# Optimization experiments

Hardware: AMD Instinct MI355X
Metric: run time of the kernel (lower is better)

Reference implementation:

```python
import jax, jax.numpy as jnp
import numpy as np

N_USERS = 10000
N_ITEMS = 40000
HID = 64
NNZ = 2_000_000
B = 8192
N_TOT = N_USERS + N_ITEMS
HOP = 3


def setup_inputs() -> dict:
    key = jax.random.key(0)
    ks = jax.random.split(key, 13)
    emb = lambda k, n: jax.random.normal(k, (n, HID), dtype=jnp.float32) * (1.0 / np.sqrt(HID))
    # Dense social adjacency; scaled so repeated propagation stays numerically stable
    S = jax.random.uniform(ks[6], (N_USERS, N_USERS), dtype=jnp.float32) * (2.0 / N_USERS)
    return {
        "users": jax.random.randint(ks[0], (B,), 0, N_USERS),
        "pos": jax.random.randint(ks[1], (B,), 0, N_ITEMS),
        "neg": jax.random.randint(ks[2], (B,), 0, N_ITEMS),
        "user_embs": emb(ks[3], N_USERS),
        "item_embs": emb(ks[4], N_ITEMS),
        "user1_embs": emb(ks[5], N_USERS),
        "item1_embs": emb(ks[7], N_ITEMS),
        "user2_embs": emb(ks[8], N_USERS),
        "item2_embs": emb(ks[9], N_ITEMS),
        "S": S,
        "A_rows": jax.random.randint(ks[10], (NNZ,), 0, N_TOT, dtype=jnp.int32),
        "A_cols": jax.random.randint(ks[11], (NNZ,), 0, N_TOT, dtype=jnp.int32),
        "A_vals": jax.random.uniform(ks[12], (NNZ,), dtype=jnp.float32) * (1.0 / 40.0),
        "hop": HOP,
    }


def social_gcn(uemb, S, hop):
    # LightGCN-style propagation over dense social graph; mean over layers 0..hop
    h = uemb
    acc = uemb
    for _ in range(hop):
        h = S @ h                      # [n_users, hid] dense GEMM
        acc = acc + h
    return acc / (hop + 1)


def ui_gcn(uemb, iemb, rows, cols, vals, hop):
    # LightGCN over sparse bipartite user-item graph of size [N_TOT, N_TOT]
    ego = jnp.concatenate([uemb, iemb], axis=0)   # [N_TOT, hid]
    h = ego
    acc = ego
    for _ in range(hop):
        msgs = vals[:, None] * h[cols]            # gather + scale  [nnz, hid]
        h = jax.ops.segment_sum(msgs, rows, num_segments=N_TOT)
        acc = acc + h
    out = acc / (hop + 1)
    return out[:N_USERS], out[N_USERS:]


def reference(users, pos, neg, user_embs, item_embs, user1_embs, item1_embs,
              user2_embs, item2_embs, S, A_rows, A_cols, A_vals, hop):
    all_user_S = social_gcn(user_embs, S, hop)
    all_user_A, all_item = ui_gcn(user_embs, item_embs, A_rows, A_cols, A_vals, hop)
    all_user = 0.5 * all_user_S + 0.5 * all_user_A

    all_user_social = social_gcn(user1_embs, S, hop)
    all_item_social = item1_embs
    all_user_rating, all_item_rating = ui_gcn(user2_embs, item2_embs, A_rows, A_cols, A_vals, hop)

    return (all_user[users], all_item[pos], all_item[neg],
            all_user_S, all_user_A,
            all_user_social[users], all_item_social[pos], all_item_social[neg],
            all_user_rating[users], all_item_rating[pos], all_item_rating[neg])
```

## Files before the change

### kernel.cpp

```cpp
#include <hip/hip_runtime.h>

#define N_USERS 10000
#define N_ITEMS 40000
#define N_TOTAL 50000
#define HID     64
#define BATCH   8192
#define HOPS    3
#define KDIM    10000
#define KTILES  157
#define KPAD    (KTILES * 64)
#define MTILES  79
#define SPLITK  8
#define NSOC    (MTILES * SPLITK)

#define O0 0
#define O1 524288
#define O2 1048576
#define O3 1572864
#define O4 2212864
#define O5 2852864
#define O6 3377152
#define O7 3901440
#define O8 4425728
#define O9 4950016
#define O10 5474304

typedef __attribute__((ext_vector_type(8))) short short8;
typedef __attribute__((ext_vector_type(4))) float floatx4;

__device__ __forceinline__ unsigned short f32bf(float f) {
  union { float f; unsigned u; } v; v.f = f;
  unsigned r = v.u + 0x7fffu + ((v.u >> 16) & 1u);
  return (unsigned short)(r >> 16);
}

__device__ __forceinline__ short8 cvt8(floatx4 v0, floatx4 v1) {
  short8 o;
  o[0] = (short)f32bf(v0[0]); o[1] = (short)f32bf(v0[1]);
  o[2] = (short)f32bf(v0[2]); o[3] = (short)f32bf(v0[3]);
  o[4] = (short)f32bf(v1[0]); o[5] = (short)f32bf(v1[1]);
  o[6] = (short)f32bf(v1[2]); o[7] = (short)f32bf(v1[3]);
  return o;
}

__global__ __launch_bounds__(256)
void init_all(const float* __restrict__ ue, const float* __restrict__ u1,
              const float* __restrict__ ie, const float* __restrict__ u2,
              const float* __restrict__ i2, const int* __restrict__ Arows,
              int* __restrict__ counts, int nnz,
              float* __restrict__ HS0, float* __restrict__ HS1, float* __restrict__ HSacc,
              float* __restrict__ E0, float* __restrict__ Eacc) {
  int b = blockIdx.x, t = threadIdx.x;
  if (b < 2500) {
    int i = b * 256 + t;
    int r = i >> 6, c = i & 63;
    float a = ue[i], x = u1[i];
    size_t p = (size_t)r * 128 + c;
    HS0[p] = a; HS0[p + 64] = x;
    HSacc[p] = a; HSacc[p + 64] = x;
    HS1[p] = 0.f; HS1[p + 64] = 0.f;
  } else if (b < 15000) {
    int i = (b - 2500) * 256 + t;
    int r = i >> 6;
    float a, x;
    if (r < N_USERS) { a = ue[i]; x = u2[i]; }
    else             { a = ie[i - N_USERS * HID]; x = i2[i - N_USERS * HID]; }
    size_t p = (size_t)r * 128 + (i & 63);
    E0[p] = a; E0[p + 64] = x;
    Eacc[p] = a; Eacc[p + 64] = x;
  } else {
    int i = (b - 15000) * 256 + t;
    if (i < nnz) atomicAdd(&counts[Arows[i]], 1);
  }
}

__global__ void scan1(const int* __restrict__ counts, int* __restrict__ offs, int* __restrict__ bsum) {
  __shared__ int sh[256];
  int t = threadIdx.x;
  int base = blockIdx.x * 1024 + t * 4;
  int v0 = 0, v1 = 0, v2 = 0, v3 = 0;
  if (base + 0 < N_TOTAL) v0 = counts[base + 0];
  if (base + 1 < N_TOTAL) v1 = counts[base + 1];
  if (base + 2 < N_TOTAL) v2 = counts[base + 2];
  if (base + 3 < N_TOTAL) v3 = counts[base + 3];
  int s = v0 + v1 + v2 + v3;
  sh[t] = s;
  __syncthreads();
  for (int d = 1; d < 256; d <<= 1) {
    int x = (t >= d) ? sh[t - d] : 0;
    __syncthreads();
    sh[t] += x;
    __syncthreads();
  }
  int excl = sh[t] - s;
  if (t == 255) bsum[blockIdx.x] = sh[255];
  if (base + 0 < N_TOTAL) offs[base + 0] = excl; excl += v0;
  if (base + 1 < N_TOTAL) offs[base + 1] = excl; excl += v1;
  if (base + 2 < N_TOTAL) offs[base + 2] = excl; excl += v2;
  if (base + 3 < N_TOTAL) offs[base + 3] = excl;
}

__global__ void scan2(int* __restrict__ bsum, int nb) {
  __shared__ int sh[64];
  int t = threadIdx.x;
  int v = (t < nb) ? bsum[t] : 0;
  sh[t] = v;
  __syncthreads();
  for (int d = 1; d < 64; d <<= 1) {
    int x = (t >= d) ? sh[t - d] : 0;
    __syncthreads();
    sh[t] += x;
    __syncthreads();
  }
  if (t < nb) bsum[t] = sh[t] - v;
}

__device__ __forceinline__ void bfrag_dev(int t, const float* __restrict__ H,
                                          unsigned short* __restrict__ Bf,
                                          float* __restrict__ ts) {
  int k0 = t * 64;
  int tid = threadIdx.x;
#pragma unroll
  for (int i = 0; i < 8; i++) {
    int f = tid + i * 256;
    int r = f >> 5, c4 = (f & 31) * 4;
    float4 v = make_float4(0.f, 0.f, 0.f, 0.f);
    if (k0 + r < KDIM) v = *(const float4*)&H[(size_t)(k0 + r) * 128 + c4];
    *(float4*)&ts[r * 132 + c4] = v;
  }
  __syncthreads();
#pragma unroll
  for (int i = 0; i < 4; i++) {
    int c0 = tid + i * 256;
    int nt = c0 >> 7, kk = (c0 >> 6) & 1, l = c0 & 63;
    int quad = l >> 4, mq = l & 15;
    short8 o;
#pragma unroll
    for (int j = 0; j < 8; j++)
      o[j] = (short)f32bf(ts[(kk * 32 + quad * 8 + j) * 132 + nt * 16 + mq]);
    *(short8*)&Bf[(((size_t)t * 8 + nt) * 2 + kk) * 512 + l * 8] = o;
  }
}

__global__ __launch_bounds__(256)
void scan3_bf(int* __restrict__ offs, const int* __restrict__ bexcl,
              int* __restrict__ cursor, int nnz,
              const float* __restrict__ hc, unsigned short* __restrict__ Bf) {
  __shared__ __align__(16) float ts[64 * 132];
  if (blockIdx.x < 196) {
    int i = blockIdx.x * 256 + threadIdx.x;
    if (i < N_TOTAL) {
      int v = offs[i] + bexcl[i >> 10];
      offs[i] = v; cursor[i] = v;
    }
    if (i == 0) offs[N_TOTAL] = nnz;
  } else {
    bfrag_dev(blockIdx.x - 196, hc, Bf, ts);
  }
}

__global__ void scatter_csr(const int* __restrict__ rows, const int* __restrict__ cols,
                            const float* __restrict__ vals, int* __restrict__ cursor,
                            int2* __restrict__ edges, int n) {
  int i = blockIdx.x * 256 + threadIdx.x;
  if (i < n) {
    int p = atomicAdd(&cursor[rows[i]], 1);
    edges[p] = make_int2(cols[i], __float_as_int(vals[i]));
  }
}

template<int H>
__global__ __launch_bounds__(256)
void social_gemm(const float* __restrict__ S, unsigned short* __restrict__ Sbf,
                 const unsigned short* __restrict__ Bf, float* __restrict__ Cdst) {
  int tid = threadIdx.x;
  int w = tid >> 6, lane = tid & 63;
  int quad = lane >> 4, mq = lane & 15;
  int mtile = blockIdx.x % MTILES;
  int ks = blockIdx.x / MTILES;
  int m0 = mtile * 128;
  int t0 = (ks * KTILES) / SPLITK;
  int t1 = ((ks + 1) * KTILES) / SPLITK;

  floatx4 acc[2][8];
#pragma unroll
  for (int rf = 0; rf < 2; rf++)
#pragma unroll
    for (int nt = 0; nt < 8; nt++) acc[rf][nt] = (floatx4){0.f, 0.f, 0.f, 0.f};

  int r0 = m0 + w * 32 + mq;
  int r1 = r0 + 16;
  const float* sr0 = S + (size_t)r0 * KDIM;
  const float* sr1 = S + (size_t)r1 * KDIM;
  size_t sb = (((size_t)mtile * KTILES) * 8 + w * 2) * 1024 + (size_t)lane * 8;

  for (int t = t0; t < t1; ++t) {
    short8 a00, a01, a10, a11;
    size_t st = sb + (size_t)t * 8192;
    if (H == 0) {
      int kb = t * 64 + quad * 8;
      a00 = a01 = a10 = a11 = (short8){0, 0, 0, 0, 0, 0, 0, 0};
      {
        int k = kb;
        if (r0 < KDIM && k < KDIM)
          a00 = cvt8(__builtin_nontemporal_load((const floatx4*)(sr0 + k)),
                     __builtin_nontemporal_load((const floatx4*)(sr0 + k + 4)));
        k = kb + 32;
        if (r0 < KDIM && k < KDIM)
          a01 = cvt8(__builtin_nontemporal_load((const floatx4*)(sr0 + k)),
                     __builtin_nontemporal_load((const floatx4*)(sr0 + k + 4)));
        k = kb;
        if (r1 < KDIM && k < KDIM)
          a10 = cvt8(__builtin_nontemporal_load((const floatx4*)(sr1 + k)),
                     __builtin_nontemporal_load((const floatx4*)(sr1 + k + 4)));
        k = kb + 32;
        if (r1 < KDIM && k < KDIM)
          a11 = cvt8(__builtin_nontemporal_load((const floatx4*)(sr1 + k)),
                     __builtin_nontemporal_load((const floatx4*)(sr1 + k + 4)));
      }
      *(short8*)&Sbf[st]        = a00;
      *(short8*)&Sbf[st + 512]  = a01;
      *(short8*)&Sbf[st + 1024] = a10;
      *(short8*)&Sbf[st + 1536] = a11;
    } else {
      a00 = *(const short8*)&Sbf[st];
      a01 = *(const short8*)&Sbf[st + 512];
      a10 = *(const short8*)&Sbf[st + 1024];
      a11 = *(const short8*)&Sbf[st + 1536];
    }
    const unsigned short* bfb = Bf + (size_t)t * 8192 + lane * 8;
#pragma unroll
    for (int kk = 0; kk < 2; kk++) {
      short8 b[8];
#pragma unroll
      for (int nt = 0; nt < 8; nt++)
        b[nt] = *(const short8*)&bfb[((size_t)nt * 2 + kk) * 512];
      short8 ax0 = kk ? a01 : a00;
      short8 ax1 = kk ? a11 : a10;
#pragma unroll
      for (int nt = 0; nt < 8; nt++) {
        acc[0][nt] = __builtin_amdgcn_mfma_f32_16x16x32_bf16(ax0, b[nt], acc[0][nt], 0, 0, 0);
        acc[1][nt] = __builtin_amdgcn_mfma_f32_16x16x32_bf16(ax1, b[nt], acc[1][nt], 0, 0, 0);
      }
    }
  }
#pragma unroll
  for (int rf = 0; rf < 2; rf++) {
    int rb = m0 + w * 32 + rf * 16 + quad * 4;
#pragma unroll
    for (int nt = 0; nt < 8; nt++) {
      int col = nt * 16 + mq;
#pragma unroll
      for (int i = 0; i < 4; i++) {
        int r = rb + i;
        if (r < KDIM) atomicAdd(&Cdst[(size_t)r * 128 + col], acc[rf][nt][i]);
      }
    }
  }
}

template<int LAST>
__global__ __launch_bounds__(256)
void ui_hop(const int* __restrict__ offs, const int2* __restrict__ edges,
            const float* __restrict__ Ein, float* __restrict__ Eout,
            float* __restrict__ Eacc) {
  int wid = blockIdx.x * 4 + (threadIdx.x >> 6);
  int lane2 = (threadIdx.x & 63) * 2;
  const float* Einl = Ein + lane2;
  int s = offs[wid], e = offs[wid + 1];
  float ax = 0.f, ay = 0.f;
  int j = s;
  for (; j + 4 <= e; j += 4) {
    int2 e0 = edges[j], e1 = edges[j + 1], e2 = edges[j + 2], e3 = edges[j + 3];
    float2 p0 = *(const float2*)&Einl[(size_t)e0.x * 128];
    float2 p1 = *(const float2*)&Einl[(size_t)e1.x * 128];
    float2 p2 = *(const float2*)&Einl[(size_t)e2.x * 128];
    float2 p3 = *(const float2*)&Einl[(size_t)e3.x * 128];
    float w0 = __int_as_float(e0.y), w1 = __int_as_float(e1.y);
    float w2 = __int_as_float(e2.y), w3 = __int_as_float(e3.y);
    ax += w0 * p0.x + w1 * p1.x + w2 * p2.x + w3 * p3.x;
    ay += w0 * p0.y + w1 * p1.y + w2 * p2.y + w3 * p3.y;
  }
  for (; j < e; ++j) {
    int2 ed = edges[j];
    float2 p = *(const float2*)&Einl[(size_t)ed.x * 128];
    float w = __int_as_float(ed.y);
    ax += w * p.x; ay += w * p.y;
  }
  size_t op = (size_t)wid * 128 + lane2;
  if (!LAST) { float2 o; o.x = ax; o.y = ay; *(float2*)&Eout[op] = o; }
  float2 a = *(float2*)&Eacc[op];
  a.x += ax; a.y += ay;
  *(float2*)&Eacc[op] = a;
}

template<int H>
__global__ __launch_bounds__(256)
void prep_kernel(const float* __restrict__ hc, unsigned short* __restrict__ Bf,
                 float* __restrict__ HSacc, float* __restrict__ hn) {
  __shared__ __align__(16) float ts[64 * 132];
  if (blockIdx.x < KTILES) {
    bfrag_dev(blockIdx.x, hc, Bf, ts);
  } else {
    int i = (blockIdx.x - KTILES) * 256 + threadIdx.x;
    if (i < (N_USERS * 128) / 4) {
      float4 h = ((const float4*)hc)[i];
      float4 a = ((float4*)HSacc)[i];
      a.x += h.x; a.y += h.y; a.z += h.z; a.w += h.w;
      ((float4*)HSacc)[i] = a;
      if (H == 1) ((float4*)hn)[i] = make_float4(0.f, 0.f, 0.f, 0.f);
    }
  }
}

__global__ __launch_bounds__(256)
void out_kernel(const int* __restrict__ users, const int* __restrict__ pos,
                const int* __restrict__ neg, const float* __restrict__ HSacc,
                const float* __restrict__ Eacc, const float* __restrict__ item1,
                float* __restrict__ out) {
  if (blockIdx.x < 2500) {
    int i = blockIdx.x * 256 + threadIdx.x;
    int r = i >> 6, c = i & 63;
    out[O3 + i] = HSacc[(size_t)r * 128 + c] * 0.25f;
    out[O4 + i] = Eacc[(size_t)r * 128 + c] * 0.25f;
  } else {
    int b = (blockIdx.x - 2500) * 4 + (threadIdx.x >> 6);
    int lane = threadIdx.x & 63;
    int u = users[b], p = pos[b], n = neg[b];
    const float q = 0.25f;
    float us = HSacc[(size_t)u * 128 + lane] * q;
    float ua = Eacc[(size_t)u * 128 + lane] * q;
    size_t bl = (size_t)b * 64 + lane;
    out[O0 + bl]  = 0.5f * (us + ua);
    out[O1 + bl]  = Eacc[(size_t)(N_USERS + p) * 128 + lane] * q;
    out[O2 + bl]  = Eacc[(size_t)(N_USERS + n) * 128 + lane] * q;
    out[O5 + bl]  = HSacc[(size_t)u * 128 + 64 + lane] * q;
    out[O6 + bl]  = item1[(size_t)p * 64 + lane];
    out[O7 + bl]  = item1[(size_t)n * 64 + lane];
    out[O8 + bl]  = Eacc[(size_t)u * 128 + 64 + lane] * q;
    out[O9 + bl]  = Eacc[(size_t)(N_USERS + p) * 128 + 64 + lane] * q;
    out[O10 + bl] = Eacc[(size_t)(N_USERS + n) * 128 + 64 + lane] * q;
  }
}

extern "C" void kernel_launch(void* const* d_in, const int* in_sizes, int n_in,
                              void* d_out, int out_size, void* d_ws, size_t ws_size,
                              hipStream_t stream) {
  (void)n_in; (void)out_size; (void)ws_size;
  const int*   users = (const int*)d_in[0];
  const int*   pos   = (const int*)d_in[1];
  const int*   neg   = (const int*)d_in[2];
  const float* ue    = (const float*)d_in[3];
  const float* ie    = (const float*)d_in[4];
  const float* u1    = (const float*)d_in[5];
  const float* i1    = (const float*)d_in[6];
  const float* u2    = (const float*)d_in[7];
  const float* i2    = (const float*)d_in[8];
  const float* S     = (const float*)d_in[9];
  const int*   Arows = (const int*)d_in[10];
  const int*   Acols = (const int*)d_in[11];
  const float* Avals = (const float*)d_in[12];
  const int nnz = in_sizes[10];

  char* ws = (char*)d_ws;
  size_t off = 0;
  auto alloc = [&](size_t b) { size_t r = off; off += (b + 255) & ~(size_t)255; return r; };
  float* HS0   = (float*)(ws + alloc(sizeof(float) * (size_t)N_USERS * 128));
  float* HS1   = (float*)(ws + alloc(sizeof(float) * (size_t)N_USERS * 128));
  float* HSacc = (float*)(ws + alloc(sizeof(float) * (size_t)N_USERS * 128));
  unsigned short* Bf  = (unsigned short*)(ws + alloc(sizeof(short) * (size_t)KTILES * 8192));
  unsigned short* Sbf = (unsigned short*)(ws + alloc(sizeof(short) * (size_t)MTILES * KTILES * 8192));
  float* E0    = (float*)(ws + alloc(sizeof(float) * (size_t)N_TOTAL * 128));
  float* E1    = (float*)(ws + alloc(sizeof(float) * (size_t)N_TOTAL * 128));
  float* Eacc  = (float*)(ws + alloc(sizeof(float) * (size_t)N_TOTAL * 128));
  int* counts  = (int*)(ws + alloc(sizeof(int) * (N_TOTAL + 16)));
  int* offs    = (int*)(ws + alloc(sizeof(int) * (N_TOTAL + 16)));
  int* cursor  = (int*)(ws + alloc(sizeof(int) * (N_TOTAL + 16)));
  int* bsum    = (int*)(ws + alloc(sizeof(int) * 256));
  int2* edges  = (int2*)(ws + alloc(sizeof(int2) * (size_t)nnz));

  const int histB = (nnz + 255) / 256;

  hipMemsetAsync(counts, 0, sizeof(int) * (N_TOTAL + 16), stream);
  init_all<<<15000 + histB, 256, 0, stream>>>(ue, u1, ie, u2, i2, Arows, counts, nnz,
                                              HS0, HS1, HSacc, E0, Eacc);
  scan1<<<49, 256, 0, stream>>>(counts, offs, bsum);
  scan2<<<1, 64, 0, stream>>>(bsum, 49);
  scan3_bf<<<196 + KTILES, 256, 0, stream>>>(offs, bsum, cursor, nnz, HS0, Bf);
  scatter_csr<<<histB, 256, 0, stream>>>(Arows, Acols, Avals, cursor, edges, nnz);

  ui_hop<0><<<12500, 256, 0, stream>>>(offs, edges, E0, E1, Eacc);
  social_gemm<0><<<NSOC, 256, 0, stream>>>(S, Sbf, Bf, HS1);
  prep_kernel<1><<<KTILES + 1250, 256, 0, stream>>>(HS1, Bf, HSacc, HS0);
  ui_hop<0><<<12500, 256, 0, stream>>>(offs, edges, E1, E0, Eacc);
  social_gemm<1><<<NSOC, 256, 0, stream>>>(S, Sbf, Bf, HS0);
  prep_kernel<2><<<KTILES + 1250, 256, 0, stream>>>(HS0, Bf, HSacc, HS1);
  ui_hop<1><<<12500, 256, 0, stream>>>(offs, edges, E0, E1, Eacc);
  social_gemm<2><<<NSOC, 256, 0, stream>>>(S, Sbf, Bf, HSacc);

  float* out = (float*)d_out;
  out_kernel<<<2500 + 2048, 256, 0, stream>>>(users, pos, neg, HSacc, Eacc, i1, out);
}
```

Baseline: 1.521 ms.

## Store sparse-hop embeddings in bf16 and replace split-K atomics with partial buffers

The UI-graph propagation now keeps the ping-pong hop embeddings as packed bf16 pairs, which halves the bytes gathered per edge. The fp32 accumulator stays full precision. The social GEMM no longer does atomicAdd into the output. Each split-K slice writes its own partial tile, and the following prep or reduce kernel sums the partials. This also removes the zeroing of the next hop buffer. The trade-off is lower precision for the intermediate hop inputs and extra partial-buffer traffic in the reduction. A 2x unroll is also added to the GEMM k-loop.

Result: faster. 1.386 ms (-8.9%).

```diff
diff --git a/kernel.cpp b/kernel.cpp
--- a/kernel.cpp
+++ b/kernel.cpp
@@ -12,6 +12,7 @@
 #define MTILES  79
 #define SPLITK  8
 #define NSOC    (MTILES * SPLITK)
+#define CP_STRIDE ((size_t)MTILES * 16384)
 
 #define O0 0
 #define O1 524288
@@ -34,6 +35,10 @@
   return (unsigned short)(r >> 16);
 }
 
+__device__ __forceinline__ unsigned packbf2(float x, float y) {
+  return (unsigned)f32bf(x) | ((unsigned)f32bf(y) << 16);
+}
+
 __device__ __forceinline__ short8 cvt8(floatx4 v0, floatx4 v1) {
   short8 o;
   o[0] = (short)f32bf(v0[0]); o[1] = (short)f32bf(v0[1]);
@@ -48,8 +53,8 @@
               const float* __restrict__ ie, const float* __restrict__ u2,
               const float* __restrict__ i2, const int* __restrict__ Arows,
               int* __restrict__ counts, int nnz,
-              float* __restrict__ HS0, float* __restrict__ HS1, float* __restrict__ HSacc,
-              float* __restrict__ E0, float* __restrict__ Eacc) {
+              float* __restrict__ HS0, float* __restrict__ HSacc,
+              unsigned* __restrict__ Eb0, float* __restrict__ Eacc) {
   int b = blockIdx.x, t = threadIdx.x;
   if (b < 2500) {
     int i = b * 256 + t;
@@ -58,18 +63,21 @@
     size_t p = (size_t)r * 128 + c;
     HS0[p] = a; HS0[p + 64] = x;
     HSacc[p] = a; HSacc[p + 64] = x;
-    HS1[p] = 0.f; HS1[p + 64] = 0.f;
-  } else if (b < 15000) {
+  } else if (b < 8750) {
     int i = (b - 2500) * 256 + t;
-    int r = i >> 6;
-    float a, x;
-    if (r < N_USERS) { a = ue[i]; x = u2[i]; }
-    else             { a = ie[i - N_USERS * HID]; x = i2[i - N_USERS * HID]; }
-    size_t p = (size_t)r * 128 + (i & 63);
-    E0[p] = a; E0[p + 64] = x;
-    Eacc[p] = a; Eacc[p + 64] = x;
+    int r = i >> 5, c2 = (i & 31) * 2;
+    const float* srcA; const float* srcB;
+    if (r < N_USERS) { srcA = ue + (size_t)r * 64 + c2; srcB = u2 + (size_t)r * 64 + c2; }
+    else { srcA = ie + (size_t)(r - N_USERS) * 64 + c2; srcB = i2 + (size_t)(r - N_USERS) * 64 + c2; }
+    float2 a = *(const float2*)srcA;
+    float2 x = *(const float2*)srcB;
+    size_t p = (size_t)r * 128 + c2;
+    *(float2*)&Eacc[p] = a;
+    *(float2*)&Eacc[p + 64] = x;
+    Eb0[(size_t)r * 64 + (c2 >> 1)] = packbf2(a.x, a.y);
+    Eb0[(size_t)r * 64 + 32 + (c2 >> 1)] = packbf2(x.x, x.y);
   } else {
-    int i = (b - 15000) * 256 + t;
+    int i = (b - 8750) * 256 + t;
     if (i < nnz) atomicAdd(&counts[Arows[i]], 1);
   }
 }
@@ -115,9 +123,25 @@
   if (t < nb) bsum[t] = sh[t] - v;
 }
 
-__device__ __forceinline__ void bfrag_dev(int t, const float* __restrict__ H,
-                                          unsigned short* __restrict__ Bf,
-                                          float* __restrict__ ts) {
+__device__ __forceinline__ void bfrag_emit(int t, const float* __restrict__ ts,
+                                           unsigned short* __restrict__ Bf) {
+  int tid = threadIdx.x;
+#pragma unroll
+  for (int i = 0; i < 4; i++) {
+    int c0 = tid + i * 256;
+    int nt = c0 >> 7, kk = (c0 >> 6) & 1, l = c0 & 63;
+    int quad = l >> 4, mq = l & 15;
+    short8 o;
+#pragma unroll
+    for (int j = 0; j < 8; j++)
+      o[j] = (short)f32bf(ts[(kk * 32 + quad * 8 + j) * 132 + nt * 16 + mq]);
+    *(short8*)&Bf[(((size_t)t * 8 + nt) * 2 + kk) * 512 + l * 8] = o;
+  }
+}
+
+__device__ __forceinline__ void bfrag_from_h(int t, const float* __restrict__ H,
+                                             unsigned short* __restrict__ Bf,
+                                             float* __restrict__ ts) {
   int k0 = t * 64;
   int tid = threadIdx.x;
 #pragma unroll
@@ -129,17 +153,32 @@
     *(float4*)&ts[r * 132 + c4] = v;
   }
   __syncthreads();
-#pragma unroll
-  for (int i = 0; i < 4; i++) {
-    int c0 = tid + i * 256;
-    int nt = c0 >> 7, kk = (c0 >> 6) & 1, l = c0 & 63;
-    int quad = l >> 4, mq = l & 15;
-    short8 o;
-#pragma unroll
-    for (int j = 0; j < 8; j++)
-      o[j] = (short)f32bf(ts[(kk * 32 + quad * 8 + j) * 132 + nt * 16 + mq]);
-    *(short8*)&Bf[(((size_t)t * 8 + nt) * 2 + kk) * 512 + l * 8] = o;
-  }
+  bfrag_emit(t, ts, Bf);
+}
+
+__device__ __forceinline__ void bfrag_from_parts(int t, const float* __restrict__ Cpart,
+                                                 unsigned short* __restrict__ Bf,
+                                                 float* __restrict__ ts) {
+  int k0 = t * 64;
+  int tid = threadIdx.x;
+#pragma unroll
+  for (int i = 0; i < 8; i++) {
+    int f = tid + i * 256;
+    int r = f >> 5, c4 = (f & 31) * 4;
+    float4 v = make_float4(0.f, 0.f, 0.f, 0.f);
+    int gk = k0 + r;
+    if (gk < KDIM) {
+      const float* p = Cpart + (size_t)(gk >> 7) * 16384 + (size_t)(gk & 127) * 128 + c4;
+#pragma unroll
+      for (int ks = 0; ks < SPLITK; ks++) {
+        float4 q = *(const float4*)p; p += CP_STRIDE;
+        v.x += q.x; v.y += q.y; v.z += q.z; v.w += q.w;
+      }
+    }
+    *(float4*)&ts[r * 132 + c4] = v;
+  }
+  __syncthreads();
+  bfrag_emit(t, ts, Bf);
 }
 
 __global__ __launch_bounds__(256)
@@ -155,7 +194,7 @@
     }
     if (i == 0) offs[N_TOTAL] = nnz;
   } else {
-    bfrag_dev(blockIdx.x - 196, hc, Bf, ts);
+    bfrag_from_h(blockIdx.x - 196, hc, Bf, ts);
   }
 }
 
@@ -169,10 +208,10 @@
   }
 }
 
-template<int H>
+template<int FIRST>
 __global__ __launch_bounds__(256)
 void social_gemm(const float* __restrict__ S, unsigned short* __restrict__ Sbf,
-                 const unsigned short* __restrict__ Bf, float* __restrict__ Cdst) {
+                 const unsigned short* __restrict__ Bf, float* __restrict__ Cpart) {
   int tid = threadIdx.x;
   int w = tid >> 6, lane = tid & 63;
   int quad = lane >> 4, mq = lane & 15;
@@ -194,10 +233,11 @@
   const float* sr1 = S + (size_t)r1 * KDIM;
   size_t sb = (((size_t)mtile * KTILES) * 8 + w * 2) * 1024 + (size_t)lane * 8;
 
+#pragma unroll 2
   for (int t = t0; t < t1; ++t) {
     short8 a00, a01, a10, a11;
     size_t st = sb + (size_t)t * 8192;
-    if (H == 0) {
+    if (FIRST) {
       int kb = t * 64 + quad * 8;
       a00 = a01 = a10 = a11 = (short8){0, 0, 0, 0, 0, 0, 0, 0};
       {
@@ -244,17 +284,16 @@
       }
     }
   }
+  float* cp = Cpart + ((size_t)ks * MTILES + mtile) * 16384;
 #pragma unroll
   for (int rf = 0; rf < 2; rf++) {
-    int rb = m0 + w * 32 + rf * 16 + quad * 4;
 #pragma unroll
     for (int nt = 0; nt < 8; nt++) {
       int col = nt * 16 + mq;
-#pragma unroll
-      for (int i = 0; i < 4; i++) {
-        int r = rb + i;
-        if (r < KDIM) atomicAdd(&Cdst[(size_t)r * 128 + col], acc[rf][nt][i]);
-      }
+      int rb = w * 32 + rf * 16 + quad * 4;
+#pragma unroll
+      for (int i = 0; i < 4; i++)
+        cp[(size_t)(rb + i) * 128 + col] = acc[rf][nt][i];
     }
   }
 }
@@ -262,54 +301,80 @@
 template<int LAST>
 __global__ __launch_bounds__(256)
 void ui_hop(const int* __restrict__ offs, const int2* __restrict__ edges,
-            const float* __restrict__ Ein, float* __restrict__ Eout,
+            const unsigned* __restrict__ Ebin, unsigned* __restrict__ Ebout,
             float* __restrict__ Eacc) {
   int wid = blockIdx.x * 4 + (threadIdx.x >> 6);
-  int lane2 = (threadIdx.x & 63) * 2;
-  const float* Einl = Ein + lane2;
+  int lane = threadIdx.x & 63;
+  const unsigned* Einl = Ebin + lane;
   int s = offs[wid], e = offs[wid + 1];
   float ax = 0.f, ay = 0.f;
   int j = s;
   for (; j + 4 <= e; j += 4) {
     int2 e0 = edges[j], e1 = edges[j + 1], e2 = edges[j + 2], e3 = edges[j + 3];
-    float2 p0 = *(const float2*)&Einl[(size_t)e0.x * 128];
-    float2 p1 = *(const float2*)&Einl[(size_t)e1.x * 128];
-    float2 p2 = *(const float2*)&Einl[(size_t)e2.x * 128];
-    float2 p3 = *(const float2*)&Einl[(size_t)e3.x * 128];
+    unsigned u0 = Einl[(size_t)e0.x * 64];
+    unsigned u1 = Einl[(size_t)e1.x * 64];
+    unsigned u2 = Einl[(size_t)e2.x * 64];
+    unsigned u3 = Einl[(size_t)e3.x * 64];
     float w0 = __int_as_float(e0.y), w1 = __int_as_float(e1.y);
     float w2 = __int_as_float(e2.y), w3 = __int_as_float(e3.y);
-    ax += w0 * p0.x + w1 * p1.x + w2 * p2.x + w3 * p3.x;
-    ay += w0 * p0.y + w1 * p1.y + w2 * p2.y + w3 * p3.y;
+    ax += w0 * __uint_as_float(u0 << 16) + w1 * __uint_as_float(u1 << 16)
+        + w2 * __uint_as_float(u2 << 16) + w3 * __uint_as_float(u3 << 16);
+    ay += w0 * __uint_as_float(u0 & 0xffff0000u) + w1 * __uint_as_float(u1 & 0xffff0000u)
+        + w2 * __uint_as_float(u2 & 0xffff0000u) + w3 * __uint_as_float(u3 & 0xffff0000u);
   }
   for (; j < e; ++j) {
     int2 ed = edges[j];
-    float2 p = *(const float2*)&Einl[(size_t)ed.x * 128];
+    unsigned u = Einl[(size_t)ed.x * 64];
     float w = __int_as_float(ed.y);
-    ax += w * p.x; ay += w * p.y;
-  }
-  size_t op = (size_t)wid * 128 + lane2;
-  if (!LAST) { float2 o; o.x = ax; o.y = ay; *(float2*)&Eout[op] = o; }
+    ax += w * __uint_as_float(u << 16);
+    ay += w * __uint_as_float(u & 0xffff0000u);
+  }
+  if (!LAST) Ebout[(size_t)wid * 64 + lane] = packbf2(ax, ay);
+  size_t op = (size_t)wid * 128 + lane * 2;
   float2 a = *(float2*)&Eacc[op];
   a.x += ax; a.y += ay;
   *(float2*)&Eacc[op] = a;
 }
 
-template<int H>
-__global__ __launch_bounds__(256)
-void prep_kernel(const float* __restrict__ hc, unsigned short* __restrict__ Bf,
-                 float* __restrict__ HSacc, float* __restrict__ hn) {
+__global__ __launch_bounds__(256)
+void prep_kernel(const float* __restrict__ Cpart, unsigned short* __restrict__ Bf,
+                 float* __restrict__ HSacc) {
   __shared__ __align__(16) float ts[64 * 132];
   if (blockIdx.x < KTILES) {
-    bfrag_dev(blockIdx.x, hc, Bf, ts);
+    bfrag_from_parts(blockIdx.x, Cpart, Bf, ts);
   } else {
     int i = (blockIdx.x - KTILES) * 256 + threadIdx.x;
     if (i < (N_USERS * 128) / 4) {
-      float4 h = ((const float4*)hc)[i];
+      int r = i >> 5, c = (i & 31) * 4;
+      const float* p = Cpart + (size_t)(r >> 7) * 16384 + (size_t)(r & 127) * 128 + c;
+      float4 v = make_float4(0.f, 0.f, 0.f, 0.f);
+#pragma unroll
+      for (int ks = 0; ks < SPLITK; ks++) {
+        float4 q = *(const float4*)p; p += CP_STRIDE;
+        v.x += q.x; v.y += q.y; v.z += q.z; v.w += q.w;
+      }
       float4 a = ((float4*)HSacc)[i];
-      a.x += h.x; a.y += h.y; a.z += h.z; a.w += h.w;
+      a.x += v.x; a.y += v.y; a.z += v.z; a.w += v.w;
       ((float4*)HSacc)[i] = a;
-      if (H == 1) ((float4*)hn)[i] = make_float4(0.f, 0.f, 0.f, 0.f);
-    }
+    }
+  }
+}
+
+__global__ __launch_bounds__(256)
+void reduce2(const float* __restrict__ Cpart, float* __restrict__ HSacc) {
+  int i = blockIdx.x * 256 + threadIdx.x;
+  if (i < (N_USERS * 128) / 4) {
+    int r = i >> 5, c = (i & 31) * 4;
+    const float* p = Cpart + (size_t)(r >> 7) * 16384 + (size_t)(r & 127) * 128 + c;
+    float4 v = make_float4(0.f, 0.f, 0.f, 0.f);
+#pragma unroll
+    for (int ks = 0; ks < SPLITK; ks++) {
+      float4 q = *(const float4*)p; p += CP_STRIDE;
+      v.x += q.x; v.y += q.y; v.z += q.z; v.w += q.w;
+    }
+    float4 a = ((float4*)HSacc)[i];
+    a.x += v.x; a.y += v.y; a.z += v.z; a.w += v.w;
+    ((float4*)HSacc)[i] = a;
   }
 }
 
@@ -366,12 +431,12 @@
   size_t off = 0;
   auto alloc = [&](size_t b) { size_t r = off; off += (b + 255) & ~(size_t)255; return r; };
   float* HS0   = (float*)(ws + alloc(sizeof(float) * (size_t)N_USERS * 128));
-  float* HS1   = (float*)(ws + alloc(sizeof(float) * (size_t)N_USERS * 128));
   float* HSacc = (float*)(ws + alloc(sizeof(float) * (size_t)N_USERS * 128));
   unsigned short* Bf  = (unsigned short*)(ws + alloc(sizeof(short) * (size_t)KTILES * 8192));
   unsigned short* Sbf = (unsigned short*)(ws + alloc(sizeof(short) * (size_t)MTILES * KTILES * 8192));
-  float* E0    = (float*)(ws + alloc(sizeof(float) * (size_t)N_TOTAL * 128));
-  float* E1    = (float*)(ws + alloc(sizeof(float) * (size_t)N_TOTAL * 128));
+  float* Cpart = (float*)(ws + alloc(sizeof(float) * (size_t)SPLITK * CP_STRIDE));
+  unsigned* Eb0 = (unsigned*)(ws + alloc(sizeof(unsigned) * (size_t)N_TOTAL * 64));
+  unsigned* Eb1 = (unsigned*)(ws + alloc(sizeof(unsigned) * (size_t)N_TOTAL * 64));
   float* Eacc  = (float*)(ws + alloc(sizeof(float) * (size_t)N_TOTAL * 128));
   int* counts  = (int*)(ws + alloc(sizeof(int) * (N_TOTAL + 16)));
   int* offs    = (int*)(ws + alloc(sizeof(int) * (N_TOTAL + 16)));
@@ -382,21 +447,22 @@
   const int histB = (nnz + 255) / 256;
 
   hipMemsetAsync(counts, 0, sizeof(int) * (N_TOTAL + 16), stream);
-  init_all<<<15000 + histB, 256, 0, stream>>>(ue, u1, ie, u2, i2, Arows, counts, nnz,
-                                              HS0, HS1, HSacc, E0, Eacc);
+  init_all<<<8750 + histB, 256, 0, stream>>>(ue, u1, ie, u2, i2, Arows, counts, nnz,
+                                             HS0, HSacc, Eb0, Eacc);
   scan1<<<49, 256, 0, stream>>>(counts, offs, bsum);
   scan2<<<1, 64, 0, stream>>>(bsum, 49);
   scan3_bf<<<196 + KTILES, 256, 0, stream>>>(offs, bsum, cursor, nnz, HS0, Bf);
   scatter_csr<<<histB, 256, 0, stream>>>(Arows, Acols, Avals, cursor, edges, nnz);
 
-  ui_hop<0><<<12500, 256, 0, stream>>>(offs, edges, E0, E1, Eacc);
-  social_gemm<0><<<NSOC, 256, 0, stream>>>(S, Sbf, Bf, HS1);
-  prep_kernel<1><<<KTILES + 1250, 256, 0, stream>>>(HS1, Bf, HSacc, HS0);
-  ui_hop<0><<<12500, 256, 0, stream>>>(offs, edges, E1, E0, Eacc);
-  social_gemm<1><<<NSOC, 256, 0, stream>>>(S, Sbf, Bf, HS0);
-  prep_kernel<2><<<KTILES + 1250, 256, 0, stream>>>(HS0, Bf, HSacc, HS1);
-  ui_hop<1><<<12500, 256, 0, stream>>>(offs, edges, E0, E1, Eacc);
-  social_gemm<2><<<NSOC, 256, 0, stream>>>(S, Sbf, Bf, HSacc);
+  ui_hop<0><<<12500, 256, 0, stream>>>(offs, edges, Eb0, Eb1, Eacc);
+  social_gemm<1><<<NSOC, 256, 0, stream>>>(S, Sbf, Bf, Cpart);
+  prep_kernel<<<KTILES + 1250, 256, 0, stream>>>(Cpart, Bf, HSacc);
+  ui_hop<0><<<12500, 256, 0, stream>>>(offs, edges, Eb1, Eb0, Eacc);
+  social_gemm<0><<<NSOC, 256, 0, stream>>>(S, Sbf, Bf, Cpart);
+  prep_kernel<<<KTILES + 1250, 256, 0, stream>>>(Cpart, Bf, HSacc);
+  ui_hop<1><<<12500, 256, 0, stream>>>(offs, edges, Eb0, Eb1, Eacc);
+  social_gemm<0><<<NSOC, 256, 0, stream>>>(S, Sbf, Bf, Cpart);
+  reduce2<<<1250, 256, 0, stream>>>(Cpart, HSacc);
 
   float* out = (float*)d_out;
   out_kernel<<<2500 + 2048, 256, 0, stream>>>(users, pos, neg, HSacc, Eacc, i1, out);
```
